# Kernel optimization log

Hardware: AMD Instinct MI355X
Metric: run time of the kernel (lower is better)

Reference implementation:

```python
import jax, jax.numpy as jnp
import numpy as np

GH, GW = 64, 64     # patch grid
WH, WW = 8, 8       # window size
NH = 8              # num heads
EMB = 128
HD = EMB // NH      # head dim = 16
M = WH * WW         # tokens per window = 64


def _masks():
    # Faithful to the torch code: row_mask blocks cross-shift attention for the
    # last window-row; column_mask is its einops-rearranged counterpart.
    half = WH * (WW // 2)
    row = np.zeros((M, M), np.float32)
    row[-half:, :-half] = -np.inf
    row[:-half, -half:] = -np.inf
    r, c = M // WH, M // WW
    # '(r wh) (c ww) -> (wh r) (ww c)'
    col = row.reshape(r, WH, c, WW).transpose(1, 0, 3, 2).reshape(M, M)
    return jnp.asarray(row), jnp.asarray(col)


def _rel_idx():
    hh, ww_ = np.meshgrid(np.arange(WH), np.arange(WW), indexing='ij')
    coords = np.stack([hh.ravel(), ww_.ravel()], -1)        # (M, 2)
    rel = coords[:, None, :] - coords[None, :, :]           # (M, M, 2)
    return jnp.asarray(rel[..., 0] + WH - 1), jnp.asarray(rel[..., 1] + WW - 1)


def setup_inputs() -> dict:
    key = jax.random.key(0)
    ks = jax.random.split(key, 4)
    B, L = 32, GH * GW
    return {
        'x': jax.random.normal(ks[0], (B, L, EMB), jnp.float32),
        'w1': jax.random.normal(ks[1], (3 * EMB, EMB), jnp.float32) * 0.02,
        'b1': jnp.zeros((3 * EMB,), jnp.float32),
        'w2': jax.random.normal(ks[2], (EMB, EMB), jnp.float32) * 0.02,
        'b2': jnp.zeros((EMB,), jnp.float32),
        'rel_bias': jax.random.normal(ks[3], (2 * WH - 1, 2 * WW - 1), jnp.float32) * 0.02,
    }


def reference(x, w1, b1, w2, b2, rel_bias):
    B, L, C = x.shape
    qkv = x @ w1.T + b1                                   # (B, L, 3C)
    # 'b (h w) (c k) -> b h w c k'  (k=3 varies fastest within channel)
    qkv = qkv.reshape(B, GH, GW, C, 3)
    # cyclic shift by half window
    qkv = jnp.roll(qkv, (-WH // 2, -WW // 2), axis=(1, 2))
    # 'b (Hw wh) (Ww ww) (e H) k -> b H Hw Ww (wh ww) e k'  (head idx fastest in C)
    qkv = qkv.reshape(B, GH // WH, WH, GW // WW, WW, HD, NH, 3)
    qkv = jnp.transpose(qkv, (0, 6, 1, 3, 2, 4, 5, 7))    # b H Hw Ww wh ww e k
    qkv = qkv.reshape(B, NH, GH // WH, GW // WW, M, HD, 3)
    Q, K, V = qkv[..., 0], qkv[..., 1], qkv[..., 2]
    wei = jnp.einsum('bhijqe,bhijke->bhijqk', Q, K) / float(np.sqrt(HD))
    ih, iw = _rel_idx()
    wei = wei + rel_bias[ih, iw]                          # (M, M) bias broadcast
    row_mask, col_mask = _masks()
    wei = wei.at[:, :, -1, :].add(row_mask)               # last window-row
    wei = wei.at[:, :, :, -1].add(col_mask)               # last window-col
    attn = jax.nn.softmax(wei, axis=-1)
    out = jnp.einsum('bhijqk,bhijke->bhijqe', attn, V)    # b H Hw Ww M e
    # 'b H Hw Ww (wh ww) e -> b (Hw wh) (Ww ww) (H e)' then flatten spatial
    out = out.reshape(B, NH, GH // WH, GW // WW, WH, WW, HD)
    out = jnp.transpose(out, (0, 2, 4, 3, 5, 1, 6)).reshape(B, L, C)
    return out @ w2.T + b2
```

## Files before the change

kernel.cpp:

```cpp
#include <hip/hip_runtime.h>
#include <math.h>

typedef _Float16 h2  __attribute__((ext_vector_type(2)));
typedef _Float16 h4  __attribute__((ext_vector_type(4)));
typedef _Float16 h8  __attribute__((ext_vector_type(8)));
typedef float    f4  __attribute__((ext_vector_type(4)));
typedef float    f32x4 __attribute__((ext_vector_type(4)));

#define W1_ELEMS (384*128)
#define W2_ELEMS (128*128)
#define LOG2E 1.44269504f

static __device__ __forceinline__ h2 pkrtz(float a, float b) {
    auto r = __builtin_amdgcn_cvt_pkrtz(a, b);
    h2 out;
    __builtin_memcpy(&out, &r, sizeof(out));
    return out;
}

static __device__ __forceinline__ h4 pkrtz4(f4 v) {
    h2 a = pkrtz(v[0], v[1]);
    h2 b = pkrtz(v[2], v[3]);
    h4 r; r[0] = a[0]; r[1] = a[1]; r[2] = b[0]; r[3] = b[1];
    return r;
}

__global__ void cvt_weights(const float* __restrict__ w1, const float* __restrict__ w2,
                            _Float16* __restrict__ w1h, _Float16* __restrict__ w2h) {
    int i = blockIdx.x * 256 + threadIdx.x;
    if (i < W1_ELEMS) w1h[i] = (_Float16)w1[i];
    if (i < W2_ELEMS) w2h[i] = (_Float16)w2[i];
}

__global__ __launch_bounds__(512, 4)
void swin_fused(const float* __restrict__ x,
                const float* __restrict__ b1,
                const float* __restrict__ b2,
                const float* __restrict__ rel_bias,
                const _Float16* __restrict__ w1h,
                const _Float16* __restrict__ w2h,
                float* __restrict__ out)
{
    __shared__ __align__(16) _Float16 xh[64*136];
    __shared__ __align__(16) _Float16 Qt[8*16*68];
    __shared__ __align__(16) _Float16 Kt[8*16*68];
    __shared__ __align__(16) _Float16 Vt[8*16*68];
    __shared__ __align__(16) _Float16 bmT[64*68];

    const int tid  = threadIdx.x;
    const int lane = tid & 63;
    const int wv   = tid >> 6;
    const int quad = lane >> 4;
    const int l16  = lane & 15;

    const int blk = blockIdx.x;
    const int b   = blk >> 6;
    const int Hw  = (blk >> 3) & 7;
    const int Ww  = blk & 7;

    {
        const int r0 = tid >> 5;
        const int c4 = tid & 31;
        for (int it = 0; it < 4; ++it) {
            int t  = r0 + it*16;
            int gi = (Hw*8 + (t >> 3) + 4) & 63;
            int gj = (Ww*8 + (t & 7) + 4) & 63;
            f32x4 v = *(const f32x4*)(x + ((size_t)b*4096 + gi*64 + gj)*128 + c4*4);
            h4 hv;
            hv[0] = (_Float16)v[0]; hv[1] = (_Float16)v[1];
            hv[2] = (_Float16)v[2]; hv[3] = (_Float16)v[3];
            *(h4*)(&xh[t*136 + c4*4]) = hv;
        }
    }
    {
        const int rowm = (Hw == 7);
        const int colm = (Ww == 7);
        for (int it = 0; it < 8; ++it) {
            int f = tid + it*512;
            int i = f >> 6, j = f & 63;
            int hi = i >> 3, wi = i & 7, hj = j >> 3, wj = j & 7;
            float v = rel_bias[(hi - hj + 7)*15 + (wi - wj + 7)] * LOG2E;
            if (rowm && ((i ^ j) & 32)) v = -INFINITY;
            if (colm && ((i ^ j) & 4))  v = -INFINITY;
            bmT[i*68 + j] = (_Float16)v;
        }
    }
    __syncthreads();

    {
        f4 acc[3][4];
        for (int cc = 0; cc < 3; ++cc)
            for (int tt = 0; tt < 4; ++tt)
                acc[cc][tt] = (f4){0.f,0.f,0.f,0.f};

        for (int kb = 0; kb < 4; ++kb) {
            h8 bfx[4];
            for (int tt = 0; tt < 4; ++tt)
                bfx[tt] = *(const h8*)(&xh[(tt*16 + l16)*136 + kb*32 + quad*8]);
            for (int cc = 0; cc < 3; ++cc) {
                int j = (wv*3 + cc)*16 + l16;
                h8 afw = *(const h8*)(w1h + (size_t)j*128 + kb*32 + quad*8);
                for (int tt = 0; tt < 4; ++tt)
                    acc[cc][tt] = __builtin_amdgcn_mfma_f32_16x16x32_f16(afw, bfx[tt], acc[cc][tt], 0, 0, 0);
            }
        }

        for (int cc = 0; cc < 3; ++cc) {
            int jq = (wv*3 + cc)*16 + quad*4;
            for (int r = 0; r < 4; ++r) {
                int j    = jq + r;
                int kind = j % 3;
                int c    = j / 3;
                int h    = c & 7;
                int e    = c >> 3;
                float bias  = b1[j];
                float scale = (kind == 0) ? 0.25f * LOG2E : 1.0f;
                _Float16* dst = (kind == 0) ? Qt : (kind == 1) ? Kt : Vt;
                dst += (h*16 + e)*68;
                for (int tt = 0; tt < 4; ++tt)
                    dst[tt*16 + l16] = (_Float16)((acc[cc][tt][r] + bias) * scale);
            }
        }
    }
    __syncthreads();

    {
        const int h = wv;
        const _Float16* Kh = &Kt[h*16*68];
        const _Float16* Qh = &Qt[h*16*68];
        const _Float16* Vh = &Vt[h*16*68];

        h4 ak[4];
        for (int mt = 0; mt < 4; ++mt)
            for (int i = 0; i < 4; ++i)
                ak[mt][i] = Kh[(quad*4 + i)*68 + mt*16 + l16];
        h4 av[4];
        for (int kt = 0; kt < 4; ++kt)
            av[kt] = *(const h4*)(Vh + l16*68 + kt*16 + quad*4);

        for (int nt = 0; nt < 4; ++nt) {
            h4 bq;
            for (int i = 0; i < 4; ++i)
                bq[i] = Qh[(quad*4 + i)*68 + nt*16 + l16];

            f4 T[4];
            for (int mt = 0; mt < 4; ++mt) {
                h4 bb = *(const h4*)(&bmT[(nt*16 + l16)*68 + mt*16 + quad*4]);
                f4 cinit;
                for (int r = 0; r < 4; ++r) cinit[r] = (float)bb[r];
                T[mt] = __builtin_amdgcn_mfma_f32_16x16x16f16(ak[mt], bq, cinit, 0, 0, 0);
            }

            float s = 0.f;
            h4 P[4];
            for (int mt = 0; mt < 4; ++mt) {
                f4 p;
                for (int r = 0; r < 4; ++r) {
                    p[r] = exp2f(T[mt][r]);
                    s += p[r];
                }
                P[mt] = pkrtz4(p);
            }
            s += __shfl_xor(s, 16, 64);
            s += __shfl_xor(s, 32, 64);
            float rcp = 1.0f / s;

            f4 o = {0.f,0.f,0.f,0.f};
            for (int kt = 0; kt < 4; ++kt)
                o = __builtin_amdgcn_mfma_f32_16x16x16f16(av[kt], P[kt], o, 0, 0, 0);
            int t = nt*16 + l16;
            f4 osc;
            for (int r = 0; r < 4; ++r) osc[r] = o[r] * rcp;
            *(h4*)(&xh[t*136 + h*16 + quad*4]) = pkrtz4(osc);
        }
    }
    __syncthreads();

    {
        h8 af[4][4];
        for (int mt = 0; mt < 4; ++mt)
            for (int kb = 0; kb < 4; ++kb)
                af[mt][kb] = *(const h8*)(&xh[(mt*16 + l16)*136 + kb*32 + quad*8]);

        int o = wv*16 + l16;
        f4 acc[4] = {{0.f,0.f,0.f,0.f},{0.f,0.f,0.f,0.f},{0.f,0.f,0.f,0.f},{0.f,0.f,0.f,0.f}};
        for (int kb = 0; kb < 4; ++kb) {
            h8 bf = *(const h8*)(w2h + (size_t)o*128 + kb*32 + quad*8);
            for (int mt = 0; mt < 4; ++mt)
                acc[mt] = __builtin_amdgcn_mfma_f32_16x16x32_f16(af[mt][kb], bf, acc[mt], 0, 0, 0);
        }
        float bias = b2[o];
        for (int mt = 0; mt < 4; ++mt) {
            for (int r = 0; r < 4; ++r) {
                int t  = mt*16 + quad*4 + r;
                int gi = Hw*8 + (t >> 3);
                int gj = Ww*8 + (t & 7);
                out[((size_t)b*4096 + gi*64 + gj)*128 + o] = acc[mt][r] + bias;
            }
        }
    }
}

extern "C" void kernel_launch(void* const* d_in, const int* in_sizes, int n_in,
                              void* d_out, int out_size, void* d_ws, size_t ws_size,
                              hipStream_t stream) {
    (void)in_sizes; (void)n_in; (void)out_size; (void)ws_size;
    const float* x  = (const float*)d_in[0];
    const float* w1 = (const float*)d_in[1];
    const float* b1 = (const float*)d_in[2];
    const float* w2 = (const float*)d_in[3];
    const float* b2 = (const float*)d_in[4];
    const float* rb = (const float*)d_in[5];

    _Float16* w1h = (_Float16*)d_ws;
    _Float16* w2h = (_Float16*)((char*)d_ws + (size_t)W1_ELEMS * sizeof(_Float16));
    float* outp = (float*)d_out;

    cvt_weights<<<(W1_ELEMS + 255)/256, 256, 0, stream>>>(w1, w2, w1h, w2h);
    swin_fused<<<32*64, 512, 0, stream>>>(x, b1, b2, rb, w1h, w2h, outp);
}
```

Baseline: 168.6 us.

## Permute QKV weights so Q/K stay in registers, precompute bias-mask tables

The prep kernel now permutes and pre-scales the rows of w1 and b1 so that each wave's QKV GEMM output lands directly in head-major Q/K/V order. Q and K are then packed straight into MFMA operand registers, and only V goes through shared memory, which drops the Qt/Kt LDS buffers, their scattered scalar stores and one barrier. The four rel-bias and mask variants are built once in global memory as fp32 tables and copied into LDS with vector loads, replacing the per-block gather. Launch bounds rise to 6 blocks per SM to use the freed LDS, at the cost of register pressure and an extra barrier around the attention-output writeback.

New measurement: 183.6 us. +8.9%, slower.

```diff
diff --git a/kernel.cpp b/kernel.cpp
--- a/kernel.cpp
+++ b/kernel.cpp
@@ -5,11 +5,13 @@
 typedef _Float16 h4  __attribute__((ext_vector_type(4)));
 typedef _Float16 h8  __attribute__((ext_vector_type(8)));
 typedef float    f4  __attribute__((ext_vector_type(4)));
-typedef float    f32x4 __attribute__((ext_vector_type(4)));
-
-#define W1_ELEMS (384*128)
-#define W2_ELEMS (128*128)
+
 #define LOG2E 1.44269504f
+#define W1P_ELEMS (384*128)
+#define W2_ELEMS  (128*128)
+#define BM_ROW    68
+#define BM_VAR    (64*BM_ROW)
+#define BM_ELEMS  (4*BM_VAR)
 
 static __device__ __forceinline__ h2 pkrtz(float a, float b) {
     auto r = __builtin_amdgcn_cvt_pkrtz(a, b);
@@ -17,7 +19,6 @@
     __builtin_memcpy(&out, &r, sizeof(out));
     return out;
 }
-
 static __device__ __forceinline__ h4 pkrtz4(f4 v) {
     h2 a = pkrtz(v[0], v[1]);
     h2 b = pkrtz(v[2], v[3]);
@@ -25,27 +26,52 @@
     return r;
 }
 
-__global__ void cvt_weights(const float* __restrict__ w1, const float* __restrict__ w2,
-                            _Float16* __restrict__ w1h, _Float16* __restrict__ w2h) {
+__global__ void prep(const float* __restrict__ w1, const float* __restrict__ b1,
+                     const float* __restrict__ w2, const float* __restrict__ rb,
+                     _Float16* __restrict__ w1p, _Float16* __restrict__ w2h,
+                     float* __restrict__ bmG, float* __restrict__ b1p)
+{
     int i = blockIdx.x * 256 + threadIdx.x;
-    if (i < W1_ELEMS) w1h[i] = (_Float16)w1[i];
+    if (i < W1P_ELEMS) {
+        int jp = i >> 7, col = i & 127;
+        int kind = jp >> 7, rem = jp & 127, h = rem >> 4, e = rem & 15;
+        int js = (e*8 + h)*3 + kind;
+        float s = (kind == 0) ? 0.25f * LOG2E : 1.0f;
+        w1p[i] = (_Float16)(w1[js*128 + col] * s);
+    }
     if (i < W2_ELEMS) w2h[i] = (_Float16)w2[i];
-}
-
-__global__ __launch_bounds__(512, 4)
+    if (i < BM_ELEMS) {
+        int v = i / BM_VAR, rem = i - v*BM_VAR;
+        int ii = rem / BM_ROW, jj = rem - ii*BM_ROW;
+        float val = 0.f;
+        if (jj < 64) {
+            int hi = ii >> 3, wi = ii & 7, hj = jj >> 3, wj = jj & 7;
+            val = rb[(hi - hj + 7)*15 + (wi - wj + 7)] * LOG2E;
+            if ((v & 2) && ((ii ^ jj) & 32)) val = -INFINITY;
+            if ((v & 1) && ((ii ^ jj) & 4))  val = -INFINITY;
+        }
+        bmG[i] = val;
+    }
+    if (i < 384) {
+        int kind = i >> 7, rem = i & 127, h = rem >> 4, e = rem & 15;
+        int js = (e*8 + h)*3 + kind;
+        float s = (kind == 0) ? 0.25f * LOG2E : 1.0f;
+        b1p[i] = b1[js] * s;
+    }
+}
+
+__global__ __launch_bounds__(512, 6)
 void swin_fused(const float* __restrict__ x,
-                const float* __restrict__ b1,
+                const float* __restrict__ b1p,
                 const float* __restrict__ b2,
-                const float* __restrict__ rel_bias,
-                const _Float16* __restrict__ w1h,
+                const _Float16* __restrict__ w1p,
                 const _Float16* __restrict__ w2h,
+                const float* __restrict__ bmG,
                 float* __restrict__ out)
 {
     __shared__ __align__(16) _Float16 xh[64*136];
-    __shared__ __align__(16) _Float16 Qt[8*16*68];
-    __shared__ __align__(16) _Float16 Kt[8*16*68];
     __shared__ __align__(16) _Float16 Vt[8*16*68];
-    __shared__ __align__(16) _Float16 bmT[64*68];
+    __shared__ __align__(16) float    bmf[64*68];
 
     const int tid  = threadIdx.x;
     const int lane = tid & 63;
@@ -65,129 +91,89 @@
             int t  = r0 + it*16;
             int gi = (Hw*8 + (t >> 3) + 4) & 63;
             int gj = (Ww*8 + (t & 7) + 4) & 63;
-            f32x4 v = *(const f32x4*)(x + ((size_t)b*4096 + gi*64 + gj)*128 + c4*4);
-            h4 hv;
-            hv[0] = (_Float16)v[0]; hv[1] = (_Float16)v[1];
-            hv[2] = (_Float16)v[2]; hv[3] = (_Float16)v[3];
-            *(h4*)(&xh[t*136 + c4*4]) = hv;
+            f4 v = *(const f4*)(x + ((size_t)b*4096 + gi*64 + gj)*128 + c4*4);
+            *(h4*)(&xh[t*136 + c4*4]) = pkrtz4(v);
         }
     }
     {
-        const int rowm = (Hw == 7);
-        const int colm = (Ww == 7);
-        for (int it = 0; it < 8; ++it) {
-            int f = tid + it*512;
-            int i = f >> 6, j = f & 63;
-            int hi = i >> 3, wi = i & 7, hj = j >> 3, wj = j & 7;
-            float v = rel_bias[(hi - hj + 7)*15 + (wi - wj + 7)] * LOG2E;
-            if (rowm && ((i ^ j) & 32)) v = -INFINITY;
-            if (colm && ((i ^ j) & 4))  v = -INFINITY;
-            bmT[i*68 + j] = (_Float16)v;
-        }
+        const float* src = bmG + ((Hw == 7 ? 2 : 0) + (Ww == 7 ? 1 : 0)) * BM_VAR;
+        for (int c = tid; c < BM_VAR/4; c += 512)
+            *(f4*)(&bmf[c*4]) = *(const f4*)(src + c*4);
     }
     __syncthreads();
 
+    f4 acc[3][4];
+    for (int cc = 0; cc < 3; ++cc)
+        for (int tt = 0; tt < 4; ++tt)
+            acc[cc][tt] = (f4){0.f, 0.f, 0.f, 0.f};
+
+    for (int kb = 0; kb < 4; ++kb) {
+        h8 bfx[4];
+        for (int tt = 0; tt < 4; ++tt)
+            bfx[tt] = *(const h8*)(&xh[(tt*16 + l16)*136 + kb*32 + quad*8]);
+        for (int cc = 0; cc < 3; ++cc) {
+            h8 afw = *(const h8*)(w1p + (size_t)(cc*128 + wv*16 + l16)*128 + kb*32 + quad*8);
+            for (int tt = 0; tt < 4; ++tt)
+                acc[cc][tt] = __builtin_amdgcn_mfma_f32_16x16x32_f16(afw, bfx[tt], acc[cc][tt], 0, 0, 0);
+        }
+    }
+
+    f4 bQ = *(const f4*)(b1p +   0 + wv*16 + quad*4);
+    f4 bK = *(const f4*)(b1p + 128 + wv*16 + quad*4);
+    f4 bV = *(const f4*)(b1p + 256 + wv*16 + quad*4);
+
+    for (int tt = 0; tt < 4; ++tt) {
+        f4 v = acc[2][tt] + bV;
+        for (int r = 0; r < 4; ++r)
+            Vt[wv*1088 + (quad*4 + r)*68 + tt*16 + l16] = (_Float16)v[r];
+    }
+
+    h4 ak[4], bq[4];
+    for (int mt = 0; mt < 4; ++mt) ak[mt] = pkrtz4(acc[1][mt] + bK);
+    for (int nt = 0; nt < 4; ++nt) bq[nt] = pkrtz4(acc[0][nt] + bQ);
+
+    h4 av[4];
+    for (int kt = 0; kt < 4; ++kt)
+        av[kt] = *(const h4*)(&Vt[wv*1088 + l16*68 + kt*16 + quad*4]);
+
+    h4 Ofrag[4];
+    for (int nt = 0; nt < 4; ++nt) {
+        f4 T[4];
+        for (int mt = 0; mt < 4; ++mt) {
+            f4 cinit = *(const f4*)(&bmf[(nt*16 + l16)*68 + mt*16 + quad*4]);
+            T[mt] = __builtin_amdgcn_mfma_f32_16x16x16f16(ak[mt], bq[nt], cinit, 0, 0, 0);
+        }
+        float s = 0.f;
+        h4 P[4];
+        for (int mt = 0; mt < 4; ++mt) {
+            f4 p;
+            for (int r = 0; r < 4; ++r) { p[r] = exp2f(T[mt][r]); s += p[r]; }
+            P[mt] = pkrtz4(p);
+        }
+        s += __shfl_xor(s, 16, 64);
+        s += __shfl_xor(s, 32, 64);
+        float rcp = 1.0f / s;
+
+        f4 o = {0.f, 0.f, 0.f, 0.f};
+        for (int kt = 0; kt < 4; ++kt)
+            o = __builtin_amdgcn_mfma_f32_16x16x16f16(av[kt], P[kt], o, 0, 0, 0);
+        Ofrag[nt] = pkrtz4(o * rcp);
+    }
+
+    __syncthreads();
+    for (int nt = 0; nt < 4; ++nt)
+        *(h4*)(&xh[(nt*16 + l16)*136 + wv*16 + quad*4]) = Ofrag[nt];
+    __syncthreads();
+
     {
-        f4 acc[3][4];
-        for (int cc = 0; cc < 3; ++cc)
-            for (int tt = 0; tt < 4; ++tt)
-                acc[cc][tt] = (f4){0.f,0.f,0.f,0.f};
-
-        for (int kb = 0; kb < 4; ++kb) {
-            h8 bfx[4];
-            for (int tt = 0; tt < 4; ++tt)
-                bfx[tt] = *(const h8*)(&xh[(tt*16 + l16)*136 + kb*32 + quad*8]);
-            for (int cc = 0; cc < 3; ++cc) {
-                int j = (wv*3 + cc)*16 + l16;
-                h8 afw = *(const h8*)(w1h + (size_t)j*128 + kb*32 + quad*8);
-                for (int tt = 0; tt < 4; ++tt)
-                    acc[cc][tt] = __builtin_amdgcn_mfma_f32_16x16x32_f16(afw, bfx[tt], acc[cc][tt], 0, 0, 0);
-            }
-        }
-
-        for (int cc = 0; cc < 3; ++cc) {
-            int jq = (wv*3 + cc)*16 + quad*4;
-            for (int r = 0; r < 4; ++r) {
-                int j    = jq + r;
-                int kind = j % 3;
-                int c    = j / 3;
-                int h    = c & 7;
-                int e    = c >> 3;
-                float bias  = b1[j];
-                float scale = (kind == 0) ? 0.25f * LOG2E : 1.0f;
-                _Float16* dst = (kind == 0) ? Qt : (kind == 1) ? Kt : Vt;
-                dst += (h*16 + e)*68;
-                for (int tt = 0; tt < 4; ++tt)
-                    dst[tt*16 + l16] = (_Float16)((acc[cc][tt][r] + bias) * scale);
-            }
-        }
-    }
-    __syncthreads();
-
-    {
-        const int h = wv;
-        const _Float16* Kh = &Kt[h*16*68];
-        const _Float16* Qh = &Qt[h*16*68];
-        const _Float16* Vh = &Vt[h*16*68];
-
-        h4 ak[4];
-        for (int mt = 0; mt < 4; ++mt)
-            for (int i = 0; i < 4; ++i)
-                ak[mt][i] = Kh[(quad*4 + i)*68 + mt*16 + l16];
-        h4 av[4];
-        for (int kt = 0; kt < 4; ++kt)
-            av[kt] = *(const h4*)(Vh + l16*68 + kt*16 + quad*4);
-
-        for (int nt = 0; nt < 4; ++nt) {
-            h4 bq;
-            for (int i = 0; i < 4; ++i)
-                bq[i] = Qh[(quad*4 + i)*68 + nt*16 + l16];
-
-            f4 T[4];
-            for (int mt = 0; mt < 4; ++mt) {
-                h4 bb = *(const h4*)(&bmT[(nt*16 + l16)*68 + mt*16 + quad*4]);
-                f4 cinit;
-                for (int r = 0; r < 4; ++r) cinit[r] = (float)bb[r];
-                T[mt] = __builtin_amdgcn_mfma_f32_16x16x16f16(ak[mt], bq, cinit, 0, 0, 0);
-            }
-
-            float s = 0.f;
-            h4 P[4];
-            for (int mt = 0; mt < 4; ++mt) {
-                f4 p;
-                for (int r = 0; r < 4; ++r) {
-                    p[r] = exp2f(T[mt][r]);
-                    s += p[r];
-                }
-                P[mt] = pkrtz4(p);
-            }
-            s += __shfl_xor(s, 16, 64);
-            s += __shfl_xor(s, 32, 64);
-            float rcp = 1.0f / s;
-
-            f4 o = {0.f,0.f,0.f,0.f};
-            for (int kt = 0; kt < 4; ++kt)
-                o = __builtin_amdgcn_mfma_f32_16x16x16f16(av[kt], P[kt], o, 0, 0, 0);
-            int t = nt*16 + l16;
-            f4 osc;
-            for (int r = 0; r < 4; ++r) osc[r] = o[r] * rcp;
-            *(h4*)(&xh[t*136 + h*16 + quad*4]) = pkrtz4(osc);
-        }
-    }
-    __syncthreads();
-
-    {
-        h8 af[4][4];
-        for (int mt = 0; mt < 4; ++mt)
-            for (int kb = 0; kb < 4; ++kb)
-                af[mt][kb] = *(const h8*)(&xh[(mt*16 + l16)*136 + kb*32 + quad*8]);
-
         int o = wv*16 + l16;
-        f4 acc[4] = {{0.f,0.f,0.f,0.f},{0.f,0.f,0.f,0.f},{0.f,0.f,0.f,0.f},{0.f,0.f,0.f,0.f}};
+        f4 acc3[4] = {{0.f,0.f,0.f,0.f},{0.f,0.f,0.f,0.f},{0.f,0.f,0.f,0.f},{0.f,0.f,0.f,0.f}};
         for (int kb = 0; kb < 4; ++kb) {
             h8 bf = *(const h8*)(w2h + (size_t)o*128 + kb*32 + quad*8);
-            for (int mt = 0; mt < 4; ++mt)
-                acc[mt] = __builtin_amdgcn_mfma_f32_16x16x32_f16(af[mt][kb], bf, acc[mt], 0, 0, 0);
+            for (int mt = 0; mt < 4; ++mt) {
+                h8 af = *(const h8*)(&xh[(mt*16 + l16)*136 + kb*32 + quad*8]);
+                acc3[mt] = __builtin_amdgcn_mfma_f32_16x16x32_f16(af, bf, acc3[mt], 0, 0, 0);
+            }
         }
         float bias = b2[o];
         for (int mt = 0; mt < 4; ++mt) {
@@ -195,7 +181,7 @@
                 int t  = mt*16 + quad*4 + r;
                 int gi = Hw*8 + (t >> 3);
                 int gj = Ww*8 + (t & 7);
-                out[((size_t)b*4096 + gi*64 + gj)*128 + o] = acc[mt][r] + bias;
+                out[((size_t)b*4096 + gi*64 + gj)*128 + o] = acc3[mt][r] + bias;
             }
         }
     }
@@ -212,10 +198,13 @@
     const float* b2 = (const float*)d_in[4];
     const float* rb = (const float*)d_in[5];
 
-    _Float16* w1h = (_Float16*)d_ws;
-    _Float16* w2h = (_Float16*)((char*)d_ws + (size_t)W1_ELEMS * sizeof(_Float16));
+    char* ws = (char*)d_ws;
+    _Float16* w1p = (_Float16*)ws;
+    _Float16* w2h = (_Float16*)(ws + 98304);
+    float*    bmG = (float*)(ws + 98304 + 32768);
+    float*    b1p = (float*)(ws + 98304 + 32768 + 69632);
     float* outp = (float*)d_out;
 
-    cvt_weights<<<(W1_ELEMS + 255)/256, 256, 0, stream>>>(w1, w2, w1h, w2h);
-    swin_fused<<<32*64, 512, 0, stream>>>(x, b1, b2, rb, w1h, w2h, outp);
-}
+    prep<<<(W1P_ELEMS + 255)/256, 256, 0, stream>>>(w1, b1, w2, rb, w1p, w2h, bmG, b1p);
+    swin_fused<<<32*64, 512, 0, stream>>>(x, b1p, b2, w1p, w2h, bmG, outp);
+}
```
